# Performance work log

Measured on AMD Instinct MI355X. Metric: run time of the kernel, lower is better.

## Reference

```python
import jax, jax.numpy as jnp
import numpy as np

B, S, D_IN, D_OUT, H = 2, 2048, 1024, 1024, 16
HD = D_OUT // H


def setup_inputs() -> dict:
    key = jax.random.key(0)
    ks = jax.random.split(key, 6)
    s_in = 1.0 / np.sqrt(D_IN)
    s_out = 1.0 / np.sqrt(D_OUT)
    return {
        "x": jax.random.normal(ks[0], (B, S, D_IN), dtype=jnp.float32),
        "wq": jax.random.uniform(ks[1], (D_IN, D_OUT), jnp.float32, -s_in, s_in),
        "wk": jax.random.uniform(ks[2], (D_IN, D_OUT), jnp.float32, -s_in, s_in),
        "wv": jax.random.uniform(ks[3], (D_IN, D_OUT), jnp.float32, -s_in, s_in),
        "wo": jax.random.uniform(ks[4], (D_OUT, D_OUT), jnp.float32, -s_out, s_out),
        "bo": jax.random.uniform(ks[5], (D_OUT,), jnp.float32, -s_out, s_out),
    }


def reference(x, wq, wk, wv, wo, bo):
    # QKV projections (qkv_bias=False)
    q = (x @ wq).reshape(B, S, H, HD)  # [B,S,H,hd]
    k = (x @ wk).reshape(B, S, H, HD)
    v = (x @ wv).reshape(B, S, H, HD)
    # scores [B,H,S,S], scaled by sqrt(head_dim)
    scores = jnp.einsum("bqhd,bkhd->bhqk", q, k) / np.sqrt(HD).astype(np.float32)
    attn = jax.nn.softmax(scores, axis=-1)  # dropout=0.0 -> no-op
    ctx = jnp.einsum("bhqk,bkhd->bqhd", attn, v).reshape(B, S, D_OUT)
    return ctx @ wo + bo
```

## Files before the change

kernel.cpp:

```cpp
#include <hip/hip_runtime.h>
#include <stdint.h>


typedef __attribute__((ext_vector_type(8))) short bf16x8;
typedef __attribute__((ext_vector_type(4))) float f32x4;

__device__ __forceinline__ unsigned short f2bf(float f) {
  unsigned u = __builtin_bit_cast(unsigned, f);
  u = (u + 0x7fffu + ((u >> 16) & 1u)) >> 16;
  return (unsigned short)u;
}
__device__ __forceinline__ float bf2f(unsigned short h) {
  unsigned u = ((unsigned)h) << 16;
  return __builtin_bit_cast(float, u);
}
__device__ __forceinline__ f32x4 mfma16(bf16x8 a, bf16x8 b, f32x4 c) {
  return __builtin_amdgcn_mfma_f32_16x16x32_bf16(a, b, c, 0, 0, 0);
}

__global__ __launch_bounds__(256) void cast_x_kernel(const float* __restrict__ x,
                                                     unsigned short* __restrict__ xb) {
  long i = (long)blockIdx.x * 256 + threadIdx.x;
  const float4* p = (const float4*)x + i * 2;
  float4 a = p[0], b = p[1];
  union { unsigned short us[8]; uint4 v; } o;
  o.us[0] = f2bf(a.x); o.us[1] = f2bf(a.y); o.us[2] = f2bf(a.z); o.us[3] = f2bf(a.w);
  o.us[4] = f2bf(b.x); o.us[5] = f2bf(b.y); o.us[6] = f2bf(b.z); o.us[7] = f2bf(b.w);
  ((uint4*)xb)[i] = o.v;
}

__global__ __launch_bounds__(256) void transpose_qkv_kernel(const float* __restrict__ wq,
    const float* __restrict__ wk, const float* __restrict__ wv,
    unsigned short* __restrict__ wqT, unsigned short* __restrict__ wkT,
    unsigned short* __restrict__ wvT) {
  const float* w = (blockIdx.z == 0) ? wq : (blockIdx.z == 1) ? wk : wv;
  unsigned short* o = (blockIdx.z == 0) ? wqT : (blockIdx.z == 1) ? wkT : wvT;
  __shared__ float t[32][33];
  int tid = threadIdx.x;
  int c = tid & 31, rr = tid >> 5;
  int k0 = blockIdx.x * 32, n0 = blockIdx.y * 32;
#pragma unroll
  for (int i = 0; i < 4; i++) t[rr + i * 8][c] = w[(size_t)(k0 + rr + i * 8) * 1024 + n0 + c];
  __syncthreads();
#pragma unroll
  for (int i = 0; i < 4; i++)
    o[(size_t)(n0 + rr + i * 8) * 1024 + k0 + c] = f2bf(t[c][rr + i * 8]);
}

__global__ __launch_bounds__(256) void transpose_wo_kernel(const float* __restrict__ w,
                                                           unsigned short* __restrict__ hi,
                                                           unsigned short* __restrict__ lo) {
  __shared__ float t[32][33];
  int tid = threadIdx.x;
  int c = tid & 31, rr = tid >> 5;
  int k0 = blockIdx.x * 32, n0 = blockIdx.y * 32;
#pragma unroll
  for (int i = 0; i < 4; i++) t[rr + i * 8][c] = w[(size_t)(k0 + rr + i * 8) * 1024 + n0 + c];
  __syncthreads();
#pragma unroll
  for (int i = 0; i < 4; i++) {
    float v = t[c][rr + i * 8];
    size_t o = (size_t)(n0 + rr + i * 8) * 1024 + k0 + c;
    unsigned short hv = f2bf(v);
    hi[o] = hv;
    lo[o] = f2bf(v - bf2f(hv));
  }
}

__device__ __forceinline__ void stage_tile64(const unsigned short* src, unsigned short* lds,
                                             int wid, int lane) {
#pragma unroll
  for (int c4 = 0; c4 < 4; ++c4) {
    int c = wid * 4 + c4;
    int row = c * 8 + (lane >> 3);
    int colb = ((lane & 7) * 16) ^ ((row & 7) << 4);
    const unsigned short* gp = src + (size_t)row * 1024 + (colb >> 1);
    __builtin_amdgcn_global_load_lds((const __attribute__((address_space(1))) void*)gp,
                                     (__attribute__((address_space(3))) void*)(lds + c * 512),
                                     16, 0, 0);
  }
}
template<int SRC_STRIDE>
__device__ __forceinline__ void stage64(const unsigned short* src, unsigned short* lds,
                                        int wid, int lane) {
#pragma unroll
  for (int c4 = 0; c4 < 2; ++c4) {
    int c = wid * 2 + c4;
    int row = c * 8 + (lane >> 3);
    int colb = ((lane & 7) * 16) ^ ((row & 7) << 4);
    const unsigned short* gp = src + (size_t)row * SRC_STRIDE + (colb >> 1);
    __builtin_amdgcn_global_load_lds((const __attribute__((address_space(1))) void*)gp,
                                     (__attribute__((address_space(3))) void*)(lds + c * 512),
                                     16, 0, 0);
  }
}
__device__ __forceinline__ bf16x8 frag_ld(const unsigned short* lds, int row, int kbyte) {
  int colb = kbyte ^ ((row & 7) << 4);
  return *(const bf16x8*)((const char*)lds + row * 128 + colb);
}

__global__ __launch_bounds__(256) void gemm_qkv_kernel(const unsigned short* __restrict__ xb,
    const unsigned short* __restrict__ wqT, const unsigned short* __restrict__ wkT,
    const unsigned short* __restrict__ wvT,
    unsigned short* __restrict__ qb, unsigned short* __restrict__ kb,
    unsigned short* __restrict__ vtb) {
  __shared__ unsigned short AS[128 * 64];
  __shared__ unsigned short BS[128 * 64];
  int tid = threadIdx.x, lane = tid & 63, wid = tid >> 6;
  int g = lane >> 4, cl = lane & 15;
  int lin = blockIdx.x + (blockIdx.y << 5) + (blockIdx.z << 8);
  int swz = (lin & 7) * 96 + (lin >> 3);
  int z = swz >> 8, rem = swz & 255;
  int m0 = (rem & 31) * 128, n0 = (rem >> 5) * 128;
  const unsigned short* wT = (z == 0) ? wqT : (z == 1) ? wkT : wvT;
  int wm = wid >> 1, wn = wid & 1;
  f32x4 acc[4][4] = {};
  for (int kt = 0; kt < 16; ++kt) {
    stage_tile64(xb + (size_t)m0 * 1024 + kt * 64, AS, wid, lane);
    stage_tile64(wT + (size_t)n0 * 1024 + kt * 64, BS, wid, lane);
    __syncthreads();
#pragma unroll
    for (int kk = 0; kk < 2; ++kk) {
      bf16x8 af[4], bfr[4];
#pragma unroll
      for (int i = 0; i < 4; ++i) af[i] = frag_ld(AS, wm * 64 + i * 16 + cl, kk * 64 + g * 16);
#pragma unroll
      for (int i = 0; i < 4; ++i) bfr[i] = frag_ld(BS, wn * 64 + i * 16 + cl, kk * 64 + g * 16);
      __builtin_amdgcn_s_setprio(1);
#pragma unroll
      for (int m = 0; m < 4; ++m)
#pragma unroll
        for (int n = 0; n < 4; ++n)
          acc[m][n] = mfma16(af[m], bfr[n], acc[m][n]);
      __builtin_amdgcn_s_setprio(0);
    }
    __syncthreads();
  }
#pragma unroll
  for (int m = 0; m < 4; ++m)
#pragma unroll
    for (int n = 0; n < 4; ++n) {
      int nn = n0 + wn * 64 + n * 16 + cl;
#pragma unroll
      for (int r = 0; r < 4; ++r) {
        int mm = m0 + wm * 64 + m * 16 + g * 4 + r;
        unsigned short val = f2bf(acc[m][n][r]);
        size_t bh = (size_t)((mm >> 11) * 16 + (nn >> 6));
        if (z < 2) {
          unsigned short* dst = (z == 0) ? qb : kb;
          dst[bh * 131072 + (size_t)(mm & 2047) * 64 + (nn & 63)] = val;
        } else {
          vtb[bh * 131072 + (size_t)(nn & 63) * 2048 + (mm & 2047)] = val;
        }
      }
    }
}

__global__ __launch_bounds__(256) void attn_kernel(const unsigned short* __restrict__ qb,
                                                   const unsigned short* __restrict__ kb,
                                                   const unsigned short* __restrict__ vtb,
                                                   unsigned short* __restrict__ ch,
                                                   unsigned short* __restrict__ clo) {
  __shared__ unsigned short Ksm[2][64 * 64];
  __shared__ unsigned short Vsm[2][64 * 64];
  __shared__ unsigned short Psm[4][32 * 72];
  int tid = threadIdx.x, lane = tid & 63, wid = tid >> 6;
  int g = lane >> 4, cl = lane & 15;
  int lin = blockIdx.x + (blockIdx.y << 4);
  int swz = (lin & 7) * 64 + (lin >> 3);
  int bh = swz >> 4;
  int q0 = (swz & 15) * 128 + wid * 32;
  size_t base = (size_t)bh * 131072;

  bf16x8 qf[2][2];
#pragma unroll
  for (int mf = 0; mf < 2; ++mf)
#pragma unroll
    for (int kk = 0; kk < 2; ++kk)
      qf[mf][kk] = *(const bf16x8*)(qb + base + (size_t)(q0 + mf * 16 + cl) * 64 + kk * 32 + g * 8);

  bf16x8 onesv;
#pragma unroll
  for (int i = 0; i < 8; ++i) onesv[i] = (short)0x3F80;

  f32x4 accO[2][4] = {};
  f32x4 accL[2] = {};

  stage64<64>(kb + base, &Ksm[0][0], wid, lane);
  stage64<2048>(vtb + base, &Vsm[0][0], wid, lane);
  __syncthreads();

  int cur = 0;
  for (int t = 0; t < 32; ++t) {
    if (t < 31) {
      stage64<64>(kb + base + (size_t)(t + 1) * 4096, &Ksm[cur ^ 1][0], wid, lane);
      stage64<2048>(vtb + base + (size_t)(t + 1) * 64, &Vsm[cur ^ 1][0], wid, lane);
    }

    f32x4 s[2][4] = {};
#pragma unroll
    for (int kk = 0; kk < 2; ++kk) {
      bf16x8 kf[4];
#pragma unroll
      for (int nf = 0; nf < 4; ++nf)
        kf[nf] = frag_ld(&Ksm[cur][0], nf * 16 + cl, kk * 64 + g * 16);
      __builtin_amdgcn_s_setprio(1);
#pragma unroll
      for (int mf = 0; mf < 2; ++mf)
#pragma unroll
        for (int nf = 0; nf < 4; ++nf)
          s[mf][nf] = mfma16(qf[mf][kk], kf[nf], s[mf][nf]);
      __builtin_amdgcn_s_setprio(0);
    }

#pragma unroll
    for (int mf = 0; mf < 2; ++mf)
#pragma unroll
      for (int r = 0; r < 4; ++r) {
        int qrow = mf * 16 + g * 4 + r;
#pragma unroll
        for (int nf = 0; nf < 4; ++nf) {
          float p = __builtin_amdgcn_exp2f(fmaf(s[mf][nf][r], 0.18033688011112042f, -8.0f));
          Psm[wid][qrow * 72 + nf * 16 + cl] = f2bf(p);
        }
      }
    __builtin_amdgcn_sched_barrier(0);

#pragma unroll
    for (int kk = 0; kk < 2; ++kk) {
      bf16x8 pa[2], vb[4];
#pragma unroll
      for (int mf = 0; mf < 2; ++mf)
        pa[mf] = *(const bf16x8*)&Psm[wid][(mf * 16 + cl) * 72 + kk * 32 + g * 8];
#pragma unroll
      for (int nf = 0; nf < 4; ++nf)
        vb[nf] = frag_ld(&Vsm[cur][0], nf * 16 + cl, kk * 64 + g * 16);
      __builtin_amdgcn_s_setprio(1);
#pragma unroll
      for (int mf = 0; mf < 2; ++mf) {
#pragma unroll
        for (int nf = 0; nf < 4; ++nf)
          accO[mf][nf] = mfma16(pa[mf], vb[nf], accO[mf][nf]);
        accL[mf] = mfma16(pa[mf], onesv, accL[mf]);
      }
      __builtin_amdgcn_s_setprio(0);
    }
    __syncthreads();
    cur ^= 1;
  }

  int b = bh >> 4, h = bh & 15;
#pragma unroll
  for (int mf = 0; mf < 2; ++mf)
#pragma unroll
    for (int r = 0; r < 4; ++r) {
      float inv = 1.0f / accL[mf][r];
      int qg = q0 + mf * 16 + g * 4 + r;
      size_t rowb = ((size_t)(b * 2048 + qg)) * 1024 + h * 64;
#pragma unroll
      for (int nf = 0; nf < 4; ++nf) {
        float o = accO[mf][nf][r] * inv;
        int d = nf * 16 + cl;
        unsigned short hv = f2bf(o);
        ch[rowb + d] = hv;
        clo[rowb + d] = f2bf(o - bf2f(hv));
      }
    }
}

__global__ __launch_bounds__(256) void gemm_out_kernel(const unsigned short* __restrict__ cah,
    const unsigned short* __restrict__ cal, const unsigned short* __restrict__ wbh,
    const unsigned short* __restrict__ wbl, const float* __restrict__ bias,
    float* __restrict__ out) {
  __shared__ unsigned short AhS[64 * 64], AlS[64 * 64];
  __shared__ unsigned short BhS[128 * 64], BlS[128 * 64];
  int tid = threadIdx.x, lane = tid & 63, wid = tid >> 6;
  int g = lane >> 4, cl = lane & 15;
  int lin = blockIdx.x + (blockIdx.y << 6);
  int swz = (lin & 7) * 64 + (lin >> 3);
  int m0 = (swz & 63) * 64, n0 = (swz >> 6) * 128;
  f32x4 acc[4][2] = {};
  for (int kt = 0; kt < 16; ++kt) {
    stage64<1024>(cah + (size_t)m0 * 1024 + kt * 64, AhS, wid, lane);
    stage64<1024>(cal + (size_t)m0 * 1024 + kt * 64, AlS, wid, lane);
    stage_tile64(wbh + (size_t)n0 * 1024 + kt * 64, BhS, wid, lane);
    stage_tile64(wbl + (size_t)n0 * 1024 + kt * 64, BlS, wid, lane);
    __syncthreads();
#pragma unroll
    for (int kk = 0; kk < 2; ++kk) {
      bf16x8 ah[4], al[4], bh[2], bl[2];
#pragma unroll
      for (int i = 0; i < 4; ++i) {
        ah[i] = frag_ld(AhS, i * 16 + cl, kk * 64 + g * 16);
        al[i] = frag_ld(AlS, i * 16 + cl, kk * 64 + g * 16);
      }
#pragma unroll
      for (int i = 0; i < 2; ++i) {
        bh[i] = frag_ld(BhS, wid * 32 + i * 16 + cl, kk * 64 + g * 16);
        bl[i] = frag_ld(BlS, wid * 32 + i * 16 + cl, kk * 64 + g * 16);
      }
      __builtin_amdgcn_s_setprio(1);
#pragma unroll
      for (int m = 0; m < 4; ++m)
#pragma unroll
        for (int n = 0; n < 2; ++n) {
          acc[m][n] = mfma16(ah[m], bh[n], acc[m][n]);
          acc[m][n] = mfma16(ah[m], bl[n], acc[m][n]);
          acc[m][n] = mfma16(al[m], bh[n], acc[m][n]);
        }
      __builtin_amdgcn_s_setprio(0);
    }
    __syncthreads();
  }
#pragma unroll
  for (int n = 0; n < 2; ++n) {
    int nn = n0 + wid * 32 + n * 16 + cl;
    float bv = bias[nn];
#pragma unroll
    for (int m = 0; m < 4; ++m)
#pragma unroll
      for (int r = 0; r < 4; ++r) {
        int mm = m0 + m * 16 + g * 4 + r;
        out[(size_t)mm * 1024 + nn] = acc[m][n][r] + bv;
      }
  }
}

extern "C" void kernel_launch(void* const* d_in, const int* in_sizes, int n_in,
                              void* d_out, int out_size, void* d_ws, size_t ws_size,
                              hipStream_t stream) {
  (void)in_sizes; (void)n_in; (void)out_size; (void)ws_size;
  const float* x  = (const float*)d_in[0];
  const float* wq = (const float*)d_in[1];
  const float* wk = (const float*)d_in[2];
  const float* wv = (const float*)d_in[3];
  const float* wo = (const float*)d_in[4];
  const float* bo = (const float*)d_in[5];
  float* out = (float*)d_out;

  char* ws = (char*)d_ws;
  unsigned short* xb   = (unsigned short*)(ws);
  unsigned short* wqT  = (unsigned short*)(ws + (8ull  << 20));
  unsigned short* wkT  = (unsigned short*)(ws + (10ull << 20));
  unsigned short* wvT  = (unsigned short*)(ws + (12ull << 20));
  unsigned short* woTh = (unsigned short*)(ws + (14ull << 20));
  unsigned short* woTl = (unsigned short*)(ws + (16ull << 20));
  unsigned short* qb   = (unsigned short*)(ws + (18ull << 20));
  unsigned short* kb   = (unsigned short*)(ws + (26ull << 20));
  unsigned short* vtb  = (unsigned short*)(ws + (34ull << 20));
  unsigned short* ch   = (unsigned short*)(ws + (42ull << 20));
  unsigned short* clo  = (unsigned short*)(ws + (50ull << 20));

  cast_x_kernel<<<2048, 256, 0, stream>>>(x, xb);
  transpose_qkv_kernel<<<dim3(32, 32, 3), 256, 0, stream>>>(wq, wk, wv, wqT, wkT, wvT);
  transpose_wo_kernel<<<dim3(32, 32), 256, 0, stream>>>(wo, woTh, woTl);
  gemm_qkv_kernel<<<dim3(32, 8, 3), 256, 0, stream>>>(xb, wqT, wkT, wvT, qb, kb, vtb);
  attn_kernel<<<dim3(16, 32), 256, 0, stream>>>(qb, kb, vtb, ch, clo);
  gemm_out_kernel<<<dim3(64, 8), 256, 0, stream>>>(ch, clo, woTh, woTl, bo, out);
}
```

Baseline: 225.7 us.

## Split attention block across eight waves with 16 query rows each

The attention kernel now runs 512 threads per block, with each wave owning 16 query rows instead of 32. K/V tile staging is spread over eight waves, one load per lane. The per-wave register footprint shrinks and more waves are available to hide latency. Each wave now reuses each K/V fragment load for less MFMA work. The probability-to-bf16 conversion also changes from round-to-nearest to plain truncation, which saves ALU ops at a small precision cost.

New measurement: 215.5 us. 4.5% less time.

```diff
diff --git a/kernel.cpp b/kernel.cpp
--- a/kernel.cpp
+++ b/kernel.cpp
@@ -93,6 +93,16 @@
                                      (__attribute__((address_space(3))) void*)(lds + c * 512),
                                      16, 0, 0);
   }
+}
+template<int SRC_STRIDE>
+__device__ __forceinline__ void stage64_8w(const unsigned short* src, unsigned short* lds,
+                                           int wid, int lane) {
+  int row = wid * 8 + (lane >> 3);
+  int colb = ((lane & 7) * 16) ^ ((row & 7) << 4);
+  const unsigned short* gp = src + (size_t)row * SRC_STRIDE + (colb >> 1);
+  __builtin_amdgcn_global_load_lds((const __attribute__((address_space(1))) void*)gp,
+                                   (__attribute__((address_space(3))) void*)(lds + wid * 512),
+                                   16, 0, 0);
 }
 __device__ __forceinline__ bf16x8 frag_ld(const unsigned short* lds, int row, int kbyte) {
   int colb = kbyte ^ ((row & 7) << 4);
@@ -156,48 +166,46 @@
     }
 }
 
-__global__ __launch_bounds__(256) void attn_kernel(const unsigned short* __restrict__ qb,
+__global__ __launch_bounds__(512) void attn_kernel(const unsigned short* __restrict__ qb,
                                                    const unsigned short* __restrict__ kb,
                                                    const unsigned short* __restrict__ vtb,
                                                    unsigned short* __restrict__ ch,
                                                    unsigned short* __restrict__ clo) {
   __shared__ unsigned short Ksm[2][64 * 64];
   __shared__ unsigned short Vsm[2][64 * 64];
-  __shared__ unsigned short Psm[4][32 * 72];
+  __shared__ unsigned short Psm[8][16 * 72];
   int tid = threadIdx.x, lane = tid & 63, wid = tid >> 6;
   int g = lane >> 4, cl = lane & 15;
   int lin = blockIdx.x + (blockIdx.y << 4);
   int swz = (lin & 7) * 64 + (lin >> 3);
   int bh = swz >> 4;
-  int q0 = (swz & 15) * 128 + wid * 32;
+  int q0 = (swz & 15) * 128 + wid * 16;
   size_t base = (size_t)bh * 131072;
 
-  bf16x8 qf[2][2];
-#pragma unroll
-  for (int mf = 0; mf < 2; ++mf)
-#pragma unroll
-    for (int kk = 0; kk < 2; ++kk)
-      qf[mf][kk] = *(const bf16x8*)(qb + base + (size_t)(q0 + mf * 16 + cl) * 64 + kk * 32 + g * 8);
+  bf16x8 qf[2];
+#pragma unroll
+  for (int kk = 0; kk < 2; ++kk)
+    qf[kk] = *(const bf16x8*)(qb + base + (size_t)(q0 + cl) * 64 + kk * 32 + g * 8);
 
   bf16x8 onesv;
 #pragma unroll
   for (int i = 0; i < 8; ++i) onesv[i] = (short)0x3F80;
 
-  f32x4 accO[2][4] = {};
-  f32x4 accL[2] = {};
-
-  stage64<64>(kb + base, &Ksm[0][0], wid, lane);
-  stage64<2048>(vtb + base, &Vsm[0][0], wid, lane);
+  f32x4 accO[4] = {};
+  f32x4 accL = {};
+
+  stage64_8w<64>(kb + base, &Ksm[0][0], wid, lane);
+  stage64_8w<2048>(vtb + base, &Vsm[0][0], wid, lane);
   __syncthreads();
 
   int cur = 0;
   for (int t = 0; t < 32; ++t) {
     if (t < 31) {
-      stage64<64>(kb + base + (size_t)(t + 1) * 4096, &Ksm[cur ^ 1][0], wid, lane);
-      stage64<2048>(vtb + base + (size_t)(t + 1) * 64, &Vsm[cur ^ 1][0], wid, lane);
-    }
-
-    f32x4 s[2][4] = {};
+      stage64_8w<64>(kb + base + (size_t)(t + 1) * 4096, &Ksm[cur ^ 1][0], wid, lane);
+      stage64_8w<2048>(vtb + base + (size_t)(t + 1) * 64, &Vsm[cur ^ 1][0], wid, lane);
+    }
+
+    f32x4 s[4] = {};
 #pragma unroll
     for (int kk = 0; kk < 2; ++kk) {
       bf16x8 kf[4];
@@ -206,43 +214,35 @@
         kf[nf] = frag_ld(&Ksm[cur][0], nf * 16 + cl, kk * 64 + g * 16);
       __builtin_amdgcn_s_setprio(1);
 #pragma unroll
-      for (int mf = 0; mf < 2; ++mf)
-#pragma unroll
-        for (int nf = 0; nf < 4; ++nf)
-          s[mf][nf] = mfma16(qf[mf][kk], kf[nf], s[mf][nf]);
+      for (int nf = 0; nf < 4; ++nf)
+        s[nf] = mfma16(qf[kk], kf[nf], s[nf]);
       __builtin_amdgcn_s_setprio(0);
     }
 
 #pragma unroll
-    for (int mf = 0; mf < 2; ++mf)
-#pragma unroll
-      for (int r = 0; r < 4; ++r) {
-        int qrow = mf * 16 + g * 4 + r;
-#pragma unroll
-        for (int nf = 0; nf < 4; ++nf) {
-          float p = __builtin_amdgcn_exp2f(fmaf(s[mf][nf][r], 0.18033688011112042f, -8.0f));
-          Psm[wid][qrow * 72 + nf * 16 + cl] = f2bf(p);
-        }
-      }
+    for (int r = 0; r < 4; ++r) {
+      int qrow = g * 4 + r;
+#pragma unroll
+      for (int nf = 0; nf < 4; ++nf) {
+        float p = __builtin_amdgcn_exp2f(fmaf(s[nf][r], 0.18033688011112042f, -8.0f));
+        Psm[wid][qrow * 72 + nf * 16 + cl] =
+            (unsigned short)(__builtin_bit_cast(unsigned, p) >> 16);
+      }
+    }
     __builtin_amdgcn_sched_barrier(0);
 
 #pragma unroll
     for (int kk = 0; kk < 2; ++kk) {
-      bf16x8 pa[2], vb[4];
-#pragma unroll
-      for (int mf = 0; mf < 2; ++mf)
-        pa[mf] = *(const bf16x8*)&Psm[wid][(mf * 16 + cl) * 72 + kk * 32 + g * 8];
+      bf16x8 pa = *(const bf16x8*)&Psm[wid][cl * 72 + kk * 32 + g * 8];
+      bf16x8 vb[4];
 #pragma unroll
       for (int nf = 0; nf < 4; ++nf)
         vb[nf] = frag_ld(&Vsm[cur][0], nf * 16 + cl, kk * 64 + g * 16);
       __builtin_amdgcn_s_setprio(1);
 #pragma unroll
-      for (int mf = 0; mf < 2; ++mf) {
-#pragma unroll
-        for (int nf = 0; nf < 4; ++nf)
-          accO[mf][nf] = mfma16(pa[mf], vb[nf], accO[mf][nf]);
-        accL[mf] = mfma16(pa[mf], onesv, accL[mf]);
-      }
+      for (int nf = 0; nf < 4; ++nf)
+        accO[nf] = mfma16(pa, vb[nf], accO[nf]);
+      accL = mfma16(pa, onesv, accL);
       __builtin_amdgcn_s_setprio(0);
     }
     __syncthreads();
@@ -251,21 +251,19 @@
 
   int b = bh >> 4, h = bh & 15;
 #pragma unroll
-  for (int mf = 0; mf < 2; ++mf)
-#pragma unroll
-    for (int r = 0; r < 4; ++r) {
-      float inv = 1.0f / accL[mf][r];
-      int qg = q0 + mf * 16 + g * 4 + r;
-      size_t rowb = ((size_t)(b * 2048 + qg)) * 1024 + h * 64;
-#pragma unroll
-      for (int nf = 0; nf < 4; ++nf) {
-        float o = accO[mf][nf][r] * inv;
-        int d = nf * 16 + cl;
-        unsigned short hv = f2bf(o);
-        ch[rowb + d] = hv;
-        clo[rowb + d] = f2bf(o - bf2f(hv));
-      }
-    }
+  for (int r = 0; r < 4; ++r) {
+    float inv = 1.0f / accL[r];
+    int qg = q0 + g * 4 + r;
+    size_t rowb = ((size_t)(b * 2048 + qg)) * 1024 + h * 64;
+#pragma unroll
+    for (int nf = 0; nf < 4; ++nf) {
+      float o = accO[nf][r] * inv;
+      int d = nf * 16 + cl;
+      unsigned short hv = f2bf(o);
+      ch[rowb + d] = hv;
+      clo[rowb + d] = f2bf(o - bf2f(hv));
+    }
+  }
 }
 
 __global__ __launch_bounds__(256) void gemm_out_kernel(const unsigned short* __restrict__ cah,
@@ -355,6 +353,6 @@
   transpose_qkv_kernel<<<dim3(32, 32, 3), 256, 0, stream>>>(wq, wk, wv, wqT, wkT, wvT);
   transpose_wo_kernel<<<dim3(32, 32), 256, 0, stream>>>(wo, woTh, woTl);
   gemm_qkv_kernel<<<dim3(32, 8, 3), 256, 0, stream>>>(xb, wqT, wkT, wvT, qb, kb, vtb);
-  attn_kernel<<<dim3(16, 32), 256, 0, stream>>>(qb, kb, vtb, ch, clo);
+  attn_kernel<<<dim3(16, 32), 512, 0, stream>>>(qb, kb, vtb, ch, clo);
   gemm_out_kernel<<<dim3(64, 8), 256, 0, stream>>>(ch, clo, woTh, woTl, bo, out);
 }
```
